# Kernel optimization log

Measured on AMD Instinct MI355X. Metric: run time of the kernel, lower is better.

Reference implementation:

```python
import jax, jax.numpy as jnp
import numpy as np

B, S, D, H, E = 4, 1024, 1024, 16, 4
HD = D // H
FF = 4 * D
EPS = 1e-5


def _ln(x):
    # normalize only; per-expert affine applied by caller
    mu = jnp.mean(x, axis=-1, keepdims=True)
    var = jnp.mean(jnp.square(x - mu), axis=-1, keepdims=True)
    return (x - mu) * jax.lax.rsqrt(var + EPS)


def setup_inputs() -> dict:
    key = jax.random.key(0)
    ks = jax.random.split(key, 12)
    s = 0.02
    inp = {
        "x": jax.random.normal(ks[0], (B, S, D), jnp.float32),
        # attention router
        "Wr_a": jax.random.normal(ks[1], (D, E), jnp.float32) * s,
        "br_a": jnp.zeros((E,), jnp.float32),
        # per-expert attention params
        "g_a": jnp.ones((E, D), jnp.float32),
        "b_a": jnp.zeros((E, D), jnp.float32),
        "Wqkv": jax.random.normal(ks[2], (E, D, 3 * D), jnp.float32) * s,
        "bqkv": jnp.zeros((E, 3 * D), jnp.float32),
        "Wpr": jax.random.normal(ks[3], (E, D, D), jnp.float32) * s,
        "bpr": jnp.zeros((E, D), jnp.float32),
        # MLP router
        "Wr_m": jax.random.normal(ks[4], (D, E), jnp.float32) * s,
        "br_m": jnp.zeros((E,), jnp.float32),
        # per-expert MLP params
        "g_m": jnp.ones((E, D), jnp.float32),
        "b_m": jnp.zeros((E, D), jnp.float32),
        "Wfc": jax.random.normal(ks[5], (E, D, FF), jnp.float32) * s,
        "bfc": jnp.zeros((E, FF), jnp.float32),
        "Wp2": jax.random.normal(ks[6], (E, FF, D), jnp.float32) * s,
        "bp2": jnp.zeros((E, D), jnp.float32),
    }
    return inp


def _block(x, Wr_a, br_a, g_a, b_a, Wqkv, bqkv, Wpr, bpr,
           Wr_m, br_m, g_m, b_m, Wfc, bfc, Wp2, bp2):
    N = B * S
    h = x.reshape(N, D)

    # ---- MoT attention (routing_all_possible_path: dense score-weighted mix) ----
    score = jax.nn.softmax(h @ Wr_a + br_a, axis=-1)          # [N,E]
    hn = _ln(h)                                                # shared normalization
    hln = hn[None, :, :] * g_a[:, None, :] + b_a[:, None, :]  # [E,N,D]
    qkv_e = jnp.einsum('end,edf->enf', hln, Wqkv) + bqkv[:, None, :]  # [E,N,3D]
    qkv = jnp.einsum('ne,enf->nf', score, qkv_e)               # [N,3D]

    q, k, v = jnp.split(qkv.reshape(B, S, 3 * D), 3, axis=-1)
    q = q.reshape(B, S, H, HD).transpose(0, 2, 1, 3)           # [B,H,S,hd]
    k = k.reshape(B, S, H, HD).transpose(0, 2, 1, 3)
    v = v.reshape(B, S, H, HD).transpose(0, 2, 1, 3)

    aw = jnp.einsum('bhqd,bhkd->bhqk', q, k) / jnp.sqrt(jnp.float32(HD))
    causal = jnp.tril(jnp.ones((S, S), bool))
    aw = jnp.where(causal, aw, jnp.finfo(aw.dtype).min)
    p = jax.nn.softmax(aw, axis=-1)
    a = jnp.einsum('bhqk,bhkd->bhqd', p, v)                    # [B,H,S,hd]
    a = a.transpose(0, 2, 1, 3).reshape(N, D)

    attn_out = jnp.einsum('ne,nd,edf->nf', score, a, Wpr) + score @ bpr
    y = x + attn_out.reshape(B, S, D)

    # ---- MoT MLP (same dense routed-expert pattern) ----
    h2 = y.reshape(N, D)
    score2 = jax.nn.softmax(h2 @ Wr_m + br_m, axis=-1)         # [N,E]
    hn2 = _ln(h2)
    hln2 = hn2[None, :, :] * g_m[:, None, :] + b_m[:, None, :]  # [E,N,D]
    inter = jax.nn.gelu(jnp.einsum('end,edf->enf', hln2, Wfc) + bfc[:, None, :])  # [E,N,FF]
    mlp_out = jnp.einsum('ne,enf,efd->nd', score2, inter, Wp2) + score2 @ bp2
    return y + mlp_out.reshape(B, S, D)


def reference(x, Wr_a, br_a, g_a, b_a, Wqkv, bqkv, Wpr, bpr,
              Wr_m, br_m, g_m, b_m, Wfc, bfc, Wp2, bp2):
    return _block(x, Wr_a, br_a, g_a, b_a, Wqkv, bqkv, Wpr, bpr,
                  Wr_m, br_m, g_m, b_m, Wfc, bfc, Wp2, bp2)
```

## Files before the change

### kernel.cpp

```cpp
#include <hip/hip_runtime.h>
#include <hip/hip_bf16.h>

typedef __bf16 bf16x8 __attribute__((ext_vector_type(8)));
typedef float f32x4 __attribute__((ext_vector_type(4)));
typedef unsigned short u16;
typedef u16 u16x8 __attribute__((ext_vector_type(8)));
typedef u16 u16x4 __attribute__((ext_vector_type(4)));

#define B_ 4
#define S_ 1024
#define D_ 1024
#define E_ 4
#define H_ 16
#define FF_ 4096
#define N_ 4096

__device__ __forceinline__ u16 f2bf(float f) {
  __hip_bfloat16 h = __float2bfloat16(f);
  return *reinterpret_cast<u16*>(&h);
}
__device__ __forceinline__ float bf2f(u16 v) {
  return __uint_as_float(((unsigned)v) << 16);
}

#define BAR()                         \
  {                                   \
    asm volatile("" ::: "memory");    \
    __builtin_amdgcn_s_barrier();     \
    asm volatile("" ::: "memory");    \
  }

__global__ __launch_bounds__(256) void tcvt(const float* __restrict__ src,
                                            u16* __restrict__ dst, int R, int C) {
  __shared__ float t[32][33];
  long base = (long)blockIdx.z * R * C;
  src += base; dst += base;
  int r0 = blockIdx.y * 32, c0 = blockIdx.x * 32;
  int tx = threadIdx.x, ty = threadIdx.y;
#pragma unroll
  for (int i = 0; i < 4; i++)
    t[ty + i * 8][tx] = src[(long)(r0 + ty + i * 8) * C + c0 + tx];
  __syncthreads();
#pragma unroll
  for (int i = 0; i < 4; i++)
    dst[(long)(c0 + ty + i * 8) * R + r0 + tx] = f2bf(t[tx][ty + i * 8]);
}

template <int YMODE, int EXPAND>
__global__ __launch_bounds__(256) void ln_router_expand(
    const float* __restrict__ X, const float* __restrict__ Wr, const float* __restrict__ br,
    const float* __restrict__ g, const float* __restrict__ bb,
    float* __restrict__ score_out, u16* __restrict__ Aout,
    long stride_e, long stride_n, int scale_flag,
    const float* __restrict__ score_a, const float* __restrict__ bpr,
    const u16* __restrict__ prt, float* __restrict__ ybuf) {
  int n = blockIdx.x, t = threadIdx.x;
  int lane = t & 63, wave = t >> 6;
  int d0 = t * 4;
  const float* xr = X + (long)n * D_;
  float4 xv = *reinterpret_cast<const float4*>(&xr[d0]);
  if (YMODE) {
    float4 sa4 = reinterpret_cast<const float4*>(score_a)[n];
    float sw[4] = {sa4.x, sa4.y, sa4.z, sa4.w};
    float4 b0 = *reinterpret_cast<const float4*>(&bpr[d0]);
    float4 b1 = *reinterpret_cast<const float4*>(&bpr[D_ + d0]);
    float4 b2 = *reinterpret_cast<const float4*>(&bpr[2 * D_ + d0]);
    float4 b3 = *reinterpret_cast<const float4*>(&bpr[3 * D_ + d0]);
    xv.x += sa4.x * b0.x + sa4.y * b1.x + sa4.z * b2.x + sa4.w * b3.x;
    xv.y += sa4.x * b0.y + sa4.y * b1.y + sa4.z * b2.y + sa4.w * b3.y;
    xv.z += sa4.x * b0.z + sa4.y * b1.z + sa4.z * b2.z + sa4.w * b3.z;
    xv.w += sa4.x * b0.w + sa4.y * b1.w + sa4.z * b2.w + sa4.w * b3.w;
    long idx = (long)n * D_ + d0;
#pragma unroll
    for (int zz = 0; zz < 4; zz++) {
      u16x4 pv = *reinterpret_cast<const u16x4*>(&prt[(long)zz * 4194304 + idx]);
      xv.x += sw[zz] * bf2f(pv[0]); xv.y += sw[zz] * bf2f(pv[1]);
      xv.z += sw[zz] * bf2f(pv[2]); xv.w += sw[zz] * bf2f(pv[3]);
    }
    *reinterpret_cast<float4*>(&ybuf[idx]) = xv;
  }
  float vals[6];
  vals[0] = xv.x + xv.y + xv.z + xv.w;
  vals[1] = xv.x * xv.x + xv.y * xv.y + xv.z * xv.z + xv.w * xv.w;
  {
    float4 w0 = reinterpret_cast<const float4*>(Wr)[d0];
    float4 w1 = reinterpret_cast<const float4*>(Wr)[d0 + 1];
    float4 w2 = reinterpret_cast<const float4*>(Wr)[d0 + 2];
    float4 w3 = reinterpret_cast<const float4*>(Wr)[d0 + 3];
    vals[2] = xv.x * w0.x + xv.y * w1.x + xv.z * w2.x + xv.w * w3.x;
    vals[3] = xv.x * w0.y + xv.y * w1.y + xv.z * w2.y + xv.w * w3.y;
    vals[4] = xv.x * w0.z + xv.y * w1.z + xv.z * w2.z + xv.w * w3.z;
    vals[5] = xv.x * w0.w + xv.y * w1.w + xv.z * w2.w + xv.w * w3.w;
  }
#pragma unroll
  for (int o = 1; o < 64; o <<= 1) {
#pragma unroll
    for (int j = 0; j < 6; j++) vals[j] += __shfl_xor(vals[j], o, 64);
  }
  __shared__ float red[4][6];
  if (lane == 0) {
#pragma unroll
    for (int j = 0; j < 6; j++) red[wave][j] = vals[j];
  }
  __syncthreads();
  float tot[6];
#pragma unroll
  for (int j = 0; j < 6; j++) tot[j] = red[0][j] + red[1][j] + red[2][j] + red[3][j];
  float mean = tot[0] * (1.0f / D_);
  float var = tot[1] * (1.0f / D_) - mean * mean;
  float rstd = rsqrtf(var + 1e-5f);
  float lg0 = tot[2] + br[0], lg1 = tot[3] + br[1], lg2 = tot[4] + br[2], lg3 = tot[5] + br[3];
  float mx = fmaxf(fmaxf(lg0, lg1), fmaxf(lg2, lg3));
  float e0 = __expf(lg0 - mx), e1 = __expf(lg1 - mx), e2 = __expf(lg2 - mx), e3 = __expf(lg3 - mx);
  float inv = 1.0f / (e0 + e1 + e2 + e3);
  float sc[4] = {e0 * inv, e1 * inv, e2 * inv, e3 * inv};
  if (t == 0) {
    float4 s4 = make_float4(sc[0], sc[1], sc[2], sc[3]);
    *reinterpret_cast<float4*>(&score_out[(long)n * 4]) = s4;
  }
  float4 hn;
  hn.x = (xv.x - mean) * rstd; hn.y = (xv.y - mean) * rstd;
  hn.z = (xv.z - mean) * rstd; hn.w = (xv.w - mean) * rstd;
  if (EXPAND) {
#pragma unroll
    for (int e = 0; e < 4; e++) {
      float4 ge = *reinterpret_cast<const float4*>(&g[e * D_ + d0]);
      float4 be = *reinterpret_cast<const float4*>(&bb[e * D_ + d0]);
      float s = scale_flag ? sc[e] : 1.0f;
      u16x4 o;
      o[0] = f2bf((hn.x * ge.x + be.x) * s);
      o[1] = f2bf((hn.y * ge.y + be.y) * s);
      o[2] = f2bf((hn.z * ge.z + be.z) * s);
      o[3] = f2bf((hn.w * ge.w + be.w) * s);
      *reinterpret_cast<u16x4*>(&Aout[(long)e * stride_e + (long)n * stride_n + d0]) = o;
    }
  } else {
    u16x4 o;
    o[0] = f2bf(hn.x); o[1] = f2bf(hn.y); o[2] = f2bf(hn.z); o[3] = f2bf(hn.w);
    *reinterpret_cast<u16x4*>(&Aout[(long)n * 1024 + d0]) = o;
  }
}

__global__ __launch_bounds__(256) void mixq(const u16* __restrict__ qp,
                                            const float* __restrict__ score_a,
                                            const float* __restrict__ bqkv,
                                            u16* __restrict__ qkvb) {
  int c = blockIdx.x * 256 + threadIdx.x;
  int n = c / 384, f0 = (c % 384) * 8;
  float4 s4 = reinterpret_cast<const float4*>(score_a)[n];
  float sw[4] = {s4.x, s4.y, s4.z, s4.w};
  float acc[8] = {};
#pragma unroll
  for (int e = 0; e < 4; e++) {
    u16x8 pv = *reinterpret_cast<const u16x8*>(&qp[(long)e * 12582912 + (long)n * 3072 + f0]);
#pragma unroll
    for (int j = 0; j < 8; j++) acc[j] += bf2f(pv[j]) + sw[e] * bqkv[e * 3072 + f0 + j];
  }
  u16x8 o;
#pragma unroll
  for (int j = 0; j < 8; j++) o[j] = f2bf(acc[j]);
  *reinterpret_cast<u16x8*>(&qkvb[(long)n * 3072 + f0]) = o;
}

template <int MODE>
__global__ __launch_bounds__(512, 2) void g8(
    const u16* __restrict__ A, const u16* __restrict__ Bt, int K, int N, int kslice,
    const float* __restrict__ score, const float* __restrict__ bias,
    u16* __restrict__ outb, int eidx, long zstride, long az, long bz) {
  __shared__ __align__(16) u16 lds0[65536];
  const int tid = threadIdx.x;
  const int w = tid >> 6, lane = tid & 63;
  const int l15 = lane & 15, l4 = lane >> 4;
  const int wr = w >> 2, wc = w & 3;

  const int gx = gridDim.x, gy = gridDim.y;
  const int total = gx * gy * gridDim.z;
  const int flat = blockIdx.x + gx * (blockIdx.y + gy * blockIdx.z);
  const int cpx = total >> 3;
  const int nf = (flat & 7) * cpx + (flat >> 3);
  const int bxi = nf % gx;
  const int tmp = nf / gx;
  const int byi = tmp % gy;
  const int z = tmp / gy;

  const long bm = (long)byi * 256, bn = (long)bxi * 256;
  const long k0 = bz ? 0L : (long)z * kslice;
  const u16* Az = bz ? (A + (long)z * az) : A;
  const u16* Btz = bz ? (Bt + (long)z * bz) : Bt;
  const int nt = kslice >> 6;

  const int cp = lane & 3;
  const int sr0 = w * 32 + (lane >> 2);
  const int sr1 = sr0 + 16;
  const int cl0 = cp ^ ((sr0 >> 1) & 3);
  const int cl1 = cp ^ ((sr1 >> 1) & 3);
  const u16* gA0 = Az + (bm + sr0) * (long)K + k0 + cl0 * 8;
  const u16* gA1 = Az + (bm + sr1) * (long)K + k0 + cl1 * 8;
  const u16* gB0 = Btz + (bn + sr0) * (long)K + k0 + cl0 * 8;
  const u16* gB1 = Btz + (bn + sr1) * (long)K + k0 + cl1 * 8;
  const int e0 = w * 1024;
  const int e1 = w * 1024 + 512;

  const int chA = l4 ^ ((l15 >> 1) & 3);
  const int rdA = (wr * 128 + l15) * 32 + chA * 8;
  const int rdB = (wc * 64 + l15) * 32 + chA * 8;

#define GLD(gsrc, ldsoff)                                                              \
  __builtin_amdgcn_global_load_lds(                                                    \
      (const __attribute__((address_space(1))) void*)(gsrc),                           \
      (__attribute__((address_space(3))) void*)(lds0 + (ldsoff)), 16, 0, 0)

  GLD(gA0, 0 + e0);
  GLD(gA1, 0 + e1);
  GLD(gB0, 16384 + e0);
  GLD(gB1, 16384 + e1);
  GLD(gA0 + 32, 8192 + e0);
  GLD(gA1 + 32, 8192 + e1);
  GLD(gB0 + 32, 24576 + e0);
  GLD(gB1 + 32, 24576 + e1);
  if (nt > 1) {
    GLD(gA0 + 64, 32768 + e0);
    GLD(gA1 + 64, 32768 + e1);
    GLD(gB0 + 64, 32768 + 16384 + e0);
    GLD(gB1 + 64, 32768 + 16384 + e1);
    GLD(gA0 + 96, 32768 + 8192 + e0);
    GLD(gA1 + 96, 32768 + 8192 + e1);
    GLD(gB0 + 96, 32768 + 24576 + e0);
    GLD(gB1 + 96, 32768 + 24576 + e1);
    asm volatile("s_waitcnt vmcnt(8)" ::: "memory");
  } else {
    asm volatile("s_waitcnt vmcnt(0)" ::: "memory");
  }
  BAR();

  f32x4 acc[8][4] = {};
  bf16x8 aC[8], bC[4], aN[8], bN[4];

#pragma unroll
  for (int i = 0; i < 8; i++) aC[i] = *(const bf16x8*)(lds0 + rdA + i * 512);
#pragma unroll
  for (int i = 0; i < 4; i++) bC[i] = *(const bf16x8*)(lds0 + 16384 + rdB + i * 512);

  for (int t = 0; t < nt; ++t) {
    const int base = (t & 1) * 32768;
    const int nb = base ^ 32768;
    const long ko2 = (long)(t + 2) * 64;
#pragma unroll
    for (int i = 0; i < 8; i++) aN[i] = *(const bf16x8*)(lds0 + base + 8192 + rdA + i * 512);
#pragma unroll
    for (int i = 0; i < 4; i++) bN[i] = *(const bf16x8*)(lds0 + base + 24576 + rdB + i * 512);
    if (t + 2 < nt) {
      GLD(gA0 + ko2, base + e0);
      GLD(gA1 + ko2, base + e1);
      GLD(gB0 + ko2, base + 16384 + e0);
      GLD(gB1 + ko2, base + 16384 + e1);
    }
    __builtin_amdgcn_s_setprio(1);
#pragma unroll
    for (int mi = 0; mi < 8; mi++)
#pragma unroll
      for (int ni = 0; ni < 4; ni++)
        acc[mi][ni] = __builtin_amdgcn_mfma_f32_16x16x32_bf16(aC[mi], bC[ni], acc[mi][ni], 0, 0, 0);
    __builtin_amdgcn_s_setprio(0);
    asm volatile("s_waitcnt lgkmcnt(0)" ::: "memory");
    if (t + 1 < nt) {
      if (t + 2 < nt) {
        asm volatile("s_waitcnt vmcnt(8)" ::: "memory");
      } else {
        asm volatile("s_waitcnt vmcnt(4)" ::: "memory");
      }
    }
    BAR();
    if (t + 1 < nt) {
#pragma unroll
      for (int i = 0; i < 8; i++) aC[i] = *(const bf16x8*)(lds0 + nb + rdA + i * 512);
#pragma unroll
      for (int i = 0; i < 4; i++) bC[i] = *(const bf16x8*)(lds0 + nb + 16384 + rdB + i * 512);
    }
    if (t + 2 < nt) {
      GLD(gA0 + ko2 + 32, base + 8192 + e0);
      GLD(gA1 + ko2 + 32, base + 8192 + e1);
      GLD(gB0 + ko2 + 32, base + 24576 + e0);
      GLD(gB1 + ko2 + 32, base + 24576 + e1);
    }
    __builtin_amdgcn_s_setprio(1);
#pragma unroll
    for (int mi = 0; mi < 8; mi++)
#pragma unroll
      for (int ni = 0; ni < 4; ni++)
        acc[mi][ni] = __builtin_amdgcn_mfma_f32_16x16x32_bf16(aN[mi], bN[ni], acc[mi][ni], 0, 0, 0);
    __builtin_amdgcn_s_setprio(0);
    asm volatile("s_waitcnt lgkmcnt(0)" ::: "memory");
    if (t + 1 < nt) {
      if (t + 2 < nt) {
        asm volatile("s_waitcnt vmcnt(8)" ::: "memory");
      } else {
        asm volatile("s_waitcnt vmcnt(0)" ::: "memory");
      }
    }
    BAR();
  }
#undef GLD

  const long zoff = (long)z * zstride;
  const int ei = bz ? z : eidx;
  const float* biasz = (MODE == 2 && bz) ? (bias + (long)z * N) : bias;
#pragma unroll
  for (int ni = 0; ni < 4; ni++) {
    long col = bn + wc * 64 + ni * 16 + l15;
    float bcol = (MODE == 2) ? biasz[col] : 0.0f;
#pragma unroll
    for (int mi = 0; mi < 8; mi++) {
#pragma unroll
      for (int r = 0; r < 4; r++) {
        long row = bm + wr * 128 + mi * 16 + l4 * 4 + r;
        float v = acc[mi][ni][r];
        if (MODE == 2) {
          float u = v + bcol;
          float zz = 0.7978845608f * (u + 0.044715f * u * u * u);
          float tt = __expf(2.0f * zz);
          float gel = u * (1.0f - 1.0f / (tt + 1.0f));
          outb[zoff + row * (long)N + col] = f2bf(gel * score[row * 4 + ei]);
        } else {
          outb[zoff + row * (long)N + col] = f2bf(v);
        }
      }
    }
  }
}

__global__ __launch_bounds__(256) void attn_kernel(const u16* __restrict__ qkv,
                                                   u16* __restrict__ aout) {
  __shared__ __align__(16) u16 Kt[32 * 64];
  __shared__ __align__(16) u16 VT[64 * 32];
  __shared__ __align__(16) u16 Pl[4][16 * 32];
  int tid = threadIdx.x, wave = tid >> 6, lane = tid & 63;
  int l15 = lane & 15, l4 = lane >> 4;
  int qblk = blockIdx.x, bh = blockIdx.y;
  int b = bh >> 4, h = bh & 15;
  int q0 = qblk * 64 + wave * 16;
  const long LD = 3072;

  bf16x8 qf[2];
  {
    const u16* qp = qkv + (long)(b * 1024 + q0 + l15) * LD + h * 64 + l4 * 8;
    qf[0] = *(const bf16x8*)qp;
    qf[1] = *(const bf16x8*)(qp + 32);
  }
  f32x4 acc[4] = {};
  float m_run = -1e30f, l_run = 0.0f;
  int kv_end = qblk * 64 + 64;

  for (int kv0 = 0; kv0 < kv_end; kv0 += 32) {
    {
      int r = tid >> 3, c = (tid & 7) * 8;
      const u16* kp = qkv + (long)(b * 1024 + kv0 + r) * LD + 1024 + h * 64 + c;
      *(u16x8*)&Kt[r * 64 + c] = *(const u16x8*)kp;
      u16x8 vv = *(const u16x8*)(kp + 1024);
#pragma unroll
      for (int j = 0; j < 8; j++) VT[(c + j) * 32 + r] = vv[j];
    }
    __syncthreads();
    if (kv0 < q0 + 16) {
      float p[8];
      float pmax = -1e30f;
      int qg = q0 + l15;
#pragma unroll
      for (int ks = 0; ks < 2; ks++) {
        f32x4 st = {};
#pragma unroll
        for (int kc = 0; kc < 2; kc++) {
          bf16x8 kf = *(const bf16x8*)&Kt[(ks * 16 + l15) * 64 + kc * 32 + l4 * 8];
          st = __builtin_amdgcn_mfma_f32_16x16x32_bf16(kf, qf[kc], st, 0, 0, 0);
        }
#pragma unroll
        for (int r = 0; r < 4; r++) {
          int kvg = kv0 + ks * 16 + l4 * 4 + r;
          float v = st[r] * 0.125f;
          if (kvg > qg) v = -1e30f;
          p[ks * 4 + r] = v;
          pmax = fmaxf(pmax, v);
        }
      }
      pmax = fmaxf(pmax, __shfl_xor(pmax, 16, 64));
      pmax = fmaxf(pmax, __shfl_xor(pmax, 32, 64));
      float m_new = fmaxf(m_run, pmax);
      float alpha = __expf(m_run - m_new);
      float rsum = 0.f;
#pragma unroll
      for (int i = 0; i < 8; i++) {
        p[i] = __expf(p[i] - m_new);
        rsum += p[i];
      }
      rsum += __shfl_xor(rsum, 16, 64);
      rsum += __shfl_xor(rsum, 32, 64);
      l_run = l_run * alpha + rsum;
      m_run = m_new;
      float af4[4];
#pragma unroll
      for (int r = 0; r < 4; r++) af4[r] = __shfl(alpha, l4 * 4 + r, 64);
#pragma unroll
      for (int i = 0; i < 4; i++) {
#pragma unroll
        for (int r = 0; r < 4; r++) acc[i][r] *= af4[r];
      }
      u16* pw = &Pl[wave][0];
#pragma unroll
      for (int i = 0; i < 8; i++) {
        int ks = i >> 2, r = i & 3;
        pw[l15 * 32 + ks * 16 + l4 * 4 + r] = f2bf(p[i]);
      }
      bf16x8 pa = *(const bf16x8*)&pw[l15 * 32 + l4 * 8];
#pragma unroll
      for (int i = 0; i < 4; i++) {
        bf16x8 vf = *(const bf16x8*)&VT[(i * 16 + l15) * 32 + l4 * 8];
        acc[i] = __builtin_amdgcn_mfma_f32_16x16x32_bf16(pa, vf, acc[i], 0, 0, 0);
      }
    }
    __syncthreads();
  }

  float linv[4];
#pragma unroll
  for (int r = 0; r < 4; r++) {
    float lv = __shfl(l_run, l4 * 4 + r, 64);
    linv[r] = 1.0f / lv;
  }
#pragma unroll
  for (int r = 0; r < 4; r++) {
    int q = l4 * 4 + r;
    long nrow = (long)b * 1024 + q0 + q;
#pragma unroll
    for (int i = 0; i < 4; i++) {
      int d = h * 64 + i * 16 + l15;
      aout[nrow * 1024 + d] = f2bf(acc[i][r] * linv[r]);
    }
  }
}

template <int FIRST>
__global__ __launch_bounds__(256) void accum_out(const float* __restrict__ ybuf,
                                                 const float* __restrict__ score_m,
                                                 const float* __restrict__ bp2,
                                                 const u16* __restrict__ p2t,
                                                 float* __restrict__ out) {
  int n = blockIdx.x, t = threadIdx.x;
  int d0 = t * 4;
  long idx = (long)n * D_ + d0;
  float4 v;
  if (FIRST) {
    float4 s4 = reinterpret_cast<const float4*>(score_m)[n];
    float4 b0 = *reinterpret_cast<const float4*>(&bp2[d0]);
    float4 b1 = *reinterpret_cast<const float4*>(&bp2[D_ + d0]);
    float4 b2 = *reinterpret_cast<const float4*>(&bp2[2 * D_ + d0]);
    float4 b3 = *reinterpret_cast<const float4*>(&bp2[3 * D_ + d0]);
    v = *reinterpret_cast<const float4*>(&ybuf[idx]);
    v.x += s4.x * b0.x + s4.y * b1.x + s4.z * b2.x + s4.w * b3.x;
    v.y += s4.x * b0.y + s4.y * b1.y + s4.z * b2.y + s4.w * b3.y;
    v.z += s4.x * b0.z + s4.y * b1.z + s4.z * b2.z + s4.w * b3.z;
    v.w += s4.x * b0.w + s4.y * b1.w + s4.z * b2.w + s4.w * b3.w;
  } else {
    v = *reinterpret_cast<const float4*>(&out[idx]);
  }
#pragma unroll
  for (int zz = 0; zz < 4; zz++) {
    u16x4 pv = *reinterpret_cast<const u16x4*>(&p2t[(long)zz * 4194304 + idx]);
    v.x += bf2f(pv[0]); v.y += bf2f(pv[1]); v.z += bf2f(pv[2]); v.w += bf2f(pv[3]);
  }
  *reinterpret_cast<float4*>(&out[idx]) = v;
}

extern "C" void kernel_launch(void* const* d_in, const int* in_sizes, int n_in, void* d_out,
                              int out_size, void* d_ws, size_t ws_size, hipStream_t stream) {
  (void)in_sizes; (void)n_in; (void)out_size; (void)ws_size;
  const float* x    = (const float*)d_in[0];
  const float* Wr_a = (const float*)d_in[1];
  const float* br_a = (const float*)d_in[2];
  const float* g_a  = (const float*)d_in[3];
  const float* b_a  = (const float*)d_in[4];
  const float* Wqkv = (const float*)d_in[5];
  const float* bqkv = (const float*)d_in[6];
  const float* Wpr  = (const float*)d_in[7];
  const float* bpr  = (const float*)d_in[8];
  const float* Wr_m = (const float*)d_in[9];
  const float* br_m = (const float*)d_in[10];
  const float* g_m  = (const float*)d_in[11];
  const float* b_m  = (const float*)d_in[12];
  const float* Wfc  = (const float*)d_in[13];
  const float* bfc  = (const float*)d_in[14];
  const float* Wp2  = (const float*)d_in[15];
  const float* bp2  = (const float*)d_in[16];
  float* out = (float*)d_out;

  char* ws = (char*)d_ws;
  const size_t MB = 1048576;
  u16* wt_q   = (u16*)(ws + 0);
  u16* wt_pr  = (u16*)(ws + 0);
  u16* wt_fc  = (u16*)(ws + 0);
  u16* A_a    = (u16*)(ws + 32 * MB);
  u16* wt_p2  = (u16*)(ws + 32 * MB);
  u16* qkvb   = (u16*)(ws + 64 * MB);
  u16* A_fc   = (u16*)(ws + 64 * MB);
  u16* p2t    = (u16*)(ws + 64 * MB);
  u16* qp     = (u16*)(ws + 96 * MB);
  u16* prt    = (u16*)(ws + 96 * MB);
  u16* inter  = (u16*)(ws + 96 * MB);
  u16* abuf   = (u16*)(ws + 192 * MB);
  float* ybuf = (float*)(ws + 224 * MB);
  float* score_a = (float*)(ws + 240 * MB);
  float* score_m = (float*)(ws + 240 * MB + 65536);

  dim3 tb(32, 8);
  tcvt<<<dim3(3072 / 32, 1024 / 32, 4), tb, 0, stream>>>(Wqkv, wt_q, 1024, 3072);
  ln_router_expand<0, 1><<<N_, 256, 0, stream>>>(x, Wr_a, br_a, g_a, b_a, score_a, A_a,
                                                 (long)4096 * 1024, (long)1024, 1,
                                                 nullptr, nullptr, nullptr, nullptr);
  g8<4><<<dim3(3072 / 256, 4096 / 256, 4), 512, 0, stream>>>(
      A_a, wt_q, 1024, 3072, 1024, nullptr, nullptr, qp, 0,
      (long)4096 * 3072, (long)4096 * 1024, (long)3072 * 1024);
  mixq<<<(4096 * 384) / 256, 256, 0, stream>>>(qp, score_a, bqkv, qkvb);
  attn_kernel<<<dim3(S_ / 64, B_ * H_), 256, 0, stream>>>(qkvb, abuf);
  tcvt<<<dim3(1024 / 32, 1024 / 32, 4), tb, 0, stream>>>(Wpr, wt_pr, 1024, 1024);
  g8<4><<<dim3(1024 / 256, 4096 / 256, 4), 512, 0, stream>>>(
      abuf, wt_pr, 1024, 1024, 1024, nullptr, nullptr, prt, 0,
      (long)4096 * 1024, 0L, (long)1024 * 1024);

  ln_router_expand<1, 1><<<N_, 256, 0, stream>>>(x, Wr_m, br_m, g_m, b_m,
                                                 score_m, A_fc, (long)N_ * 1024, (long)1024,
                                                 0, score_a, bpr, prt, ybuf);
  tcvt<<<dim3(4096 / 32, 1024 / 32, 4), tb, 0, stream>>>(Wfc, wt_fc, 1024, 4096);
  tcvt<<<dim3(1024 / 32, 4096 / 32, 4), tb, 0, stream>>>(Wp2, wt_p2, 4096, 1024);
  g8<2><<<dim3(4096 / 256, 4096 / 256, 4), 512, 0, stream>>>(
      A_fc, wt_fc, 1024, 4096, 1024, score_m, bfc, inter, 0,
      (long)4096 * 4096, (long)N_ * 1024, (long)4096 * 1024);
  g8<4><<<dim3(1024 / 256, 4096 / 256, 4), 512, 0, stream>>>(
      inter, wt_p2, 4096, 1024, 4096, nullptr, nullptr, p2t, 0,
      (long)4096 * 1024, (long)N_ * 4096, (long)1024 * 4096);
  accum_out<1><<<N_, 256, 0, stream>>>(ybuf, score_m, bp2, p2t, out);
}
```

Before: 701.5 us.

## Write GEMM outputs in contiguous 256x256 tile-blocked layout and read them tiled

The GEMM epilogue now writes each 256x256 output tile as a contiguous 128KB block instead of row-major strided rows. All consumers (mixq, ln_router_expand, accum_out) and the FC2 GEMM's A-operand loads, via a new AT template flag, switch to tiled indexing. The aim is more contiguous stores and fewer partial-line writes from the epilogue, and page-local A reads for the FF GEMM. The cost is more complex address arithmetic and strided reads in the elementwise consumer kernels.

```diff
diff --git a/kernel.cpp b/kernel.cpp
--- a/kernel.cpp
+++ b/kernel.cpp
@@ -70,14 +70,15 @@
     xv.y += sa4.x * b0.y + sa4.y * b1.y + sa4.z * b2.y + sa4.w * b3.y;
     xv.z += sa4.x * b0.z + sa4.y * b1.z + sa4.z * b2.z + sa4.w * b3.z;
     xv.w += sa4.x * b0.w + sa4.y * b1.w + sa4.z * b2.w + sa4.w * b3.w;
-    long idx = (long)n * D_ + d0;
 #pragma unroll
     for (int zz = 0; zz < 4; zz++) {
-      u16x4 pv = *reinterpret_cast<const u16x4*>(&prt[(long)zz * 4194304 + idx]);
+      long toff = ((((long)zz * 16 + (n >> 8)) * 4 + (d0 >> 8)) << 16) +
+                  (long)(n & 255) * 256 + (d0 & 255);
+      u16x4 pv = *reinterpret_cast<const u16x4*>(&prt[toff]);
       xv.x += sw[zz] * bf2f(pv[0]); xv.y += sw[zz] * bf2f(pv[1]);
       xv.z += sw[zz] * bf2f(pv[2]); xv.w += sw[zz] * bf2f(pv[3]);
     }
-    *reinterpret_cast<float4*>(&ybuf[idx]) = xv;
+    *reinterpret_cast<float4*>(&ybuf[(long)n * D_ + d0]) = xv;
   }
   float vals[6];
   vals[0] = xv.x + xv.y + xv.z + xv.w;
@@ -152,7 +153,9 @@
   float acc[8] = {};
 #pragma unroll
   for (int e = 0; e < 4; e++) {
-    u16x8 pv = *reinterpret_cast<const u16x8*>(&qp[(long)e * 12582912 + (long)n * 3072 + f0]);
+    long toff = ((((long)e * 16 + (n >> 8)) * 12 + (f0 >> 8)) << 16) +
+                (long)(n & 255) * 256 + (f0 & 255);
+    u16x8 pv = *reinterpret_cast<const u16x8*>(&qp[toff]);
 #pragma unroll
     for (int j = 0; j < 8; j++) acc[j] += bf2f(pv[j]) + sw[e] * bqkv[e * 3072 + f0 + j];
   }
@@ -162,11 +165,11 @@
   *reinterpret_cast<u16x8*>(&qkvb[(long)n * 3072 + f0]) = o;
 }
 
-template <int MODE>
+template <int MODE, int AT>
 __global__ __launch_bounds__(512, 2) void g8(
     const u16* __restrict__ A, const u16* __restrict__ Bt, int K, int N, int kslice,
     const float* __restrict__ score, const float* __restrict__ bias,
-    u16* __restrict__ outb, int eidx, long zstride, long az, long bz) {
+    u16* __restrict__ outb, long az, long bz) {
   __shared__ __align__(16) u16 lds0[65536];
   const int tid = threadIdx.x;
   const int w = tid >> 6, lane = tid & 63;
@@ -194,8 +197,15 @@
   const int sr1 = sr0 + 16;
   const int cl0 = cp ^ ((sr0 >> 1) & 3);
   const int cl1 = cp ^ ((sr1 >> 1) & 3);
-  const u16* gA0 = Az + (bm + sr0) * (long)K + k0 + cl0 * 8;
-  const u16* gA1 = Az + (bm + sr1) * (long)K + k0 + cl1 * 8;
+  const u16 *gA0, *gA1;
+  if (AT) {
+    const u16* At = Az + (((long)byi * (kslice >> 8)) << 16);
+    gA0 = At + sr0 * 256 + cl0 * 8;
+    gA1 = At + sr1 * 256 + cl1 * 8;
+  } else {
+    gA0 = Az + (bm + sr0) * (long)K + k0 + cl0 * 8;
+    gA1 = Az + (bm + sr1) * (long)K + k0 + cl1 * 8;
+  }
   const u16* gB0 = Btz + (bn + sr0) * (long)K + k0 + cl0 * 8;
   const u16* gB1 = Btz + (bn + sr1) * (long)K + k0 + cl1 * 8;
   const int e0 = w * 1024;
@@ -205,6 +215,7 @@
   const int rdA = (wr * 128 + l15) * 32 + chA * 8;
   const int rdB = (wc * 64 + l15) * 32 + chA * 8;
 
+#define KMAP(ko) (AT ? ((((long)(ko) >> 8) << 16) | ((long)(ko) & 255)) : (long)(ko))
 #define GLD(gsrc, ldsoff)                                                              \
   __builtin_amdgcn_global_load_lds(                                                    \
       (const __attribute__((address_space(1))) void*)(gsrc),                           \
@@ -214,17 +225,17 @@
   GLD(gA1, 0 + e1);
   GLD(gB0, 16384 + e0);
   GLD(gB1, 16384 + e1);
-  GLD(gA0 + 32, 8192 + e0);
-  GLD(gA1 + 32, 8192 + e1);
+  GLD(gA0 + KMAP(32), 8192 + e0);
+  GLD(gA1 + KMAP(32), 8192 + e1);
   GLD(gB0 + 32, 24576 + e0);
   GLD(gB1 + 32, 24576 + e1);
   if (nt > 1) {
-    GLD(gA0 + 64, 32768 + e0);
-    GLD(gA1 + 64, 32768 + e1);
+    GLD(gA0 + KMAP(64), 32768 + e0);
+    GLD(gA1 + KMAP(64), 32768 + e1);
     GLD(gB0 + 64, 32768 + 16384 + e0);
     GLD(gB1 + 64, 32768 + 16384 + e1);
-    GLD(gA0 + 96, 32768 + 8192 + e0);
-    GLD(gA1 + 96, 32768 + 8192 + e1);
+    GLD(gA0 + KMAP(96), 32768 + 8192 + e0);
+    GLD(gA1 + KMAP(96), 32768 + 8192 + e1);
     GLD(gB0 + 96, 32768 + 24576 + e0);
     GLD(gB1 + 96, 32768 + 24576 + e1);
     asm volatile("s_waitcnt vmcnt(8)" ::: "memory");
@@ -250,8 +261,8 @@
 #pragma unroll
     for (int i = 0; i < 4; i++) bN[i] = *(const bf16x8*)(lds0 + base + 24576 + rdB + i * 512);
     if (t + 2 < nt) {
-      GLD(gA0 + ko2, base + e0);
-      GLD(gA1 + ko2, base + e1);
+      GLD(gA0 + KMAP(ko2), base + e0);
+      GLD(gA1 + KMAP(ko2), base + e1);
       GLD(gB0 + ko2, base + 16384 + e0);
       GLD(gB1 + ko2, base + 16384 + e1);
     }
@@ -278,8 +289,8 @@
       for (int i = 0; i < 4; i++) bC[i] = *(const bf16x8*)(lds0 + nb + 16384 + rdB + i * 512);
     }
     if (t + 2 < nt) {
-      GLD(gA0 + ko2 + 32, base + 8192 + e0);
-      GLD(gA1 + ko2 + 32, base + 8192 + e1);
+      GLD(gA0 + KMAP(ko2 + 32), base + 8192 + e0);
+      GLD(gA1 + KMAP(ko2 + 32), base + 8192 + e1);
       GLD(gB0 + ko2 + 32, base + 24576 + e0);
       GLD(gB1 + ko2 + 32, base + 24576 + e1);
     }
@@ -301,29 +312,28 @@
     BAR();
   }
 #undef GLD
-
-  const long zoff = (long)z * zstride;
-  const int ei = bz ? z : eidx;
-  const float* biasz = (MODE == 2 && bz) ? (bias + (long)z * N) : bias;
+#undef KMAP
+
+  u16* outT = outb + ((((long)z * gy + byi) * gx + bxi) << 16);
+  const float* biasz = (MODE == 2) ? (bias + (long)z * N) : bias;
 #pragma unroll
   for (int ni = 0; ni < 4; ni++) {
-    long col = bn + wc * 64 + ni * 16 + l15;
-    float bcol = (MODE == 2) ? biasz[col] : 0.0f;
+    int cl = wc * 64 + ni * 16 + l15;
+    float bcol = (MODE == 2) ? biasz[bn + cl] : 0.0f;
 #pragma unroll
     for (int mi = 0; mi < 8; mi++) {
 #pragma unroll
       for (int r = 0; r < 4; r++) {
-        long row = bm + wr * 128 + mi * 16 + l4 * 4 + r;
+        int rl = wr * 128 + mi * 16 + l4 * 4 + r;
         float v = acc[mi][ni][r];
         if (MODE == 2) {
           float u = v + bcol;
           float zz = 0.7978845608f * (u + 0.044715f * u * u * u);
           float tt = __expf(2.0f * zz);
           float gel = u * (1.0f - 1.0f / (tt + 1.0f));
-          outb[zoff + row * (long)N + col] = f2bf(gel * score[row * 4 + ei]);
-        } else {
-          outb[zoff + row * (long)N + col] = f2bf(v);
+          v = gel * score[(bm + rl) * 4 + z];
         }
+        outT[rl * 256 + cl] = f2bf(v);
       }
     }
   }
@@ -438,7 +448,6 @@
   }
 }
 
-template <int FIRST>
 __global__ __launch_bounds__(256) void accum_out(const float* __restrict__ ybuf,
                                                  const float* __restrict__ score_m,
                                                  const float* __restrict__ bp2,
@@ -447,24 +456,21 @@
   int n = blockIdx.x, t = threadIdx.x;
   int d0 = t * 4;
   long idx = (long)n * D_ + d0;
-  float4 v;
-  if (FIRST) {
-    float4 s4 = reinterpret_cast<const float4*>(score_m)[n];
-    float4 b0 = *reinterpret_cast<const float4*>(&bp2[d0]);
-    float4 b1 = *reinterpret_cast<const float4*>(&bp2[D_ + d0]);
-    float4 b2 = *reinterpret_cast<const float4*>(&bp2[2 * D_ + d0]);
-    float4 b3 = *reinterpret_cast<const float4*>(&bp2[3 * D_ + d0]);
-    v = *reinterpret_cast<const float4*>(&ybuf[idx]);
-    v.x += s4.x * b0.x + s4.y * b1.x + s4.z * b2.x + s4.w * b3.x;
-    v.y += s4.x * b0.y + s4.y * b1.y + s4.z * b2.y + s4.w * b3.y;
-    v.z += s4.x * b0.z + s4.y * b1.z + s4.z * b2.z + s4.w * b3.z;
-    v.w += s4.x * b0.w + s4.y * b1.w + s4.z * b2.w + s4.w * b3.w;
-  } else {
-    v = *reinterpret_cast<const float4*>(&out[idx]);
-  }
+  float4 s4 = reinterpret_cast<const float4*>(score_m)[n];
+  float4 b0 = *reinterpret_cast<const float4*>(&bp2[d0]);
+  float4 b1 = *reinterpret_cast<const float4*>(&bp2[D_ + d0]);
+  float4 b2 = *reinterpret_cast<const float4*>(&bp2[2 * D_ + d0]);
+  float4 b3 = *reinterpret_cast<const float4*>(&bp2[3 * D_ + d0]);
+  float4 v = *reinterpret_cast<const float4*>(&ybuf[idx]);
+  v.x += s4.x * b0.x + s4.y * b1.x + s4.z * b2.x + s4.w * b3.x;
+  v.y += s4.x * b0.y + s4.y * b1.y + s4.z * b2.y + s4.w * b3.y;
+  v.z += s4.x * b0.z + s4.y * b1.z + s4.z * b2.z + s4.w * b3.z;
+  v.w += s4.x * b0.w + s4.y * b1.w + s4.z * b2.w + s4.w * b3.w;
 #pragma unroll
   for (int zz = 0; zz < 4; zz++) {
-    u16x4 pv = *reinterpret_cast<const u16x4*>(&p2t[(long)zz * 4194304 + idx]);
+    long toff = ((((long)zz * 16 + (n >> 8)) * 4 + (d0 >> 8)) << 16) +
+                (long)(n & 255) * 256 + (d0 & 255);
+    u16x4 pv = *reinterpret_cast<const u16x4*>(&p2t[toff]);
     v.x += bf2f(pv[0]); v.y += bf2f(pv[1]); v.z += bf2f(pv[2]); v.w += bf2f(pv[3]);
   }
   *reinterpret_cast<float4*>(&out[idx]) = v;
@@ -515,26 +521,26 @@
   ln_router_expand<0, 1><<<N_, 256, 0, stream>>>(x, Wr_a, br_a, g_a, b_a, score_a, A_a,
                                                  (long)4096 * 1024, (long)1024, 1,
                                                  nullptr, nullptr, nullptr, nullptr);
-  g8<4><<<dim3(3072 / 256, 4096 / 256, 4), 512, 0, stream>>>(
-      A_a, wt_q, 1024, 3072, 1024, nullptr, nullptr, qp, 0,
-      (long)4096 * 3072, (long)4096 * 1024, (long)3072 * 1024);
+  g8<4, 0><<<dim3(3072 / 256, 4096 / 256, 4), 512, 0, stream>>>(
+      A_a, wt_q, 1024, 3072, 1024, nullptr, nullptr, qp,
+      (long)4096 * 1024, (long)3072 * 1024);
   mixq<<<(4096 * 384) / 256, 256, 0, stream>>>(qp, score_a, bqkv, qkvb);
   attn_kernel<<<dim3(S_ / 64, B_ * H_), 256, 0, stream>>>(qkvb, abuf);
   tcvt<<<dim3(1024 / 32, 1024 / 32, 4), tb, 0, stream>>>(Wpr, wt_pr, 1024, 1024);
-  g8<4><<<dim3(1024 / 256, 4096 / 256, 4), 512, 0, stream>>>(
-      abuf, wt_pr, 1024, 1024, 1024, nullptr, nullptr, prt, 0,
-      (long)4096 * 1024, 0L, (long)1024 * 1024);
+  g8<4, 0><<<dim3(1024 / 256, 4096 / 256, 4), 512, 0, stream>>>(
+      abuf, wt_pr, 1024, 1024, 1024, nullptr, nullptr, prt,
+      0L, (long)1024 * 1024);
 
   ln_router_expand<1, 1><<<N_, 256, 0, stream>>>(x, Wr_m, br_m, g_m, b_m,
                                                  score_m, A_fc, (long)N_ * 1024, (long)1024,
                                                  0, score_a, bpr, prt, ybuf);
   tcvt<<<dim3(4096 / 32, 1024 / 32, 4), tb, 0, stream>>>(Wfc, wt_fc, 1024, 4096);
   tcvt<<<dim3(1024 / 32, 4096 / 32, 4), tb, 0, stream>>>(Wp2, wt_p2, 4096, 1024);
-  g8<2><<<dim3(4096 / 256, 4096 / 256, 4), 512, 0, stream>>>(
-      A_fc, wt_fc, 1024, 4096, 1024, score_m, bfc, inter, 0,
-      (long)4096 * 4096, (long)N_ * 1024, (long)4096 * 1024);
-  g8<4><<<dim3(1024 / 256, 4096 / 256, 4), 512, 0, stream>>>(
-      inter, wt_p2, 4096, 1024, 4096, nullptr, nullptr, p2t, 0,
-      (long)4096 * 1024, (long)N_ * 4096, (long)1024 * 4096);
-  accum_out<1><<<N_, 256, 0, stream>>>(ybuf, score_m, bp2, p2t, out);
-}
+  g8<2, 0><<<dim3(4096 / 256, 4096 / 256, 4), 512, 0, stream>>>(
+      A_fc, wt_fc, 1024, 4096, 1024, score_m, bfc, inter,
+      (long)N_ * 1024, (long)4096 * 1024);
+  g8<4, 1><<<dim3(1024 / 256, 4096 / 256, 4), 512, 0, stream>>>(
+      inter, wt_p2, 4096, 1024, 4096, nullptr, nullptr, p2t,
+      (long)N_ * 4096, (long)1024 * 4096);
+  accum_out<<<N_, 256, 0, stream>>>(ybuf, score_m, bp2, p2t, out);
+}
```

After: 710.8 us. No clear change (+1.3%).
